# Kernel optimization log

Hardware: AMD Instinct MI355X
Metric: run time of the kernel (lower is better)

The kernel has to match this reference:

```python
import jax, jax.numpy as jnp
import numpy as np

D_MODEL = 1024
N_HEADS = 16
HEAD_DIM = D_MODEL // N_HEADS
D_FF = 4096
EPS = 1e-5


def layer_norm(x, w, b):
    mu = jnp.mean(x, axis=-1, keepdims=True)
    var = jnp.var(x, axis=-1, keepdims=True)
    return (x - mu) * jax.lax.rsqrt(var + EPS) * w + b


def setup_inputs() -> dict:
    key = jax.random.key(0)
    ks = jax.random.split(key, 8)
    B, T, C = 2, 2048, D_MODEL
    s = lambda fan_in: 1.0 / np.sqrt(fan_in)
    return {
        "x": jax.random.normal(ks[0], (B, T, C), dtype=jnp.float32),
        "ln1_w": jnp.ones((C,), jnp.float32),
        "ln1_b": jnp.zeros((C,), jnp.float32),
        "qkv_w": jax.random.normal(ks[1], (3 * C, C), jnp.float32) * s(C),
        "attn_out_w": jax.random.normal(ks[2], (C, C), jnp.float32) * s(C),
        "ln2_w": jnp.ones((C,), jnp.float32),
        "ln2_b": jnp.zeros((C,), jnp.float32),
        "mlp_in_w": jax.random.normal(ks[3], (D_FF, C), jnp.float32) * s(C),
        "mlp_gate_w": jax.random.normal(ks[4], (D_FF, C), jnp.float32) * s(C),
        "mlp_out_w": jax.random.normal(ks[5], (C, D_FF), jnp.float32) * s(D_FF),
    }


def reference(x, ln1_w, ln1_b, qkv_w, attn_out_w, ln2_w, ln2_b,
              mlp_in_w, mlp_gate_w, mlp_out_w):
    B, T, C = x.shape
    # --- causal self-attention (pre-norm) ---
    h = layer_norm(x, ln1_w, ln1_b)
    qkv = h @ qkv_w.T  # [B,T,3C]
    q, k, v = jnp.split(qkv, 3, axis=-1)
    def heads(t):
        return t.reshape(B, T, N_HEADS, HEAD_DIM).transpose(0, 2, 1, 3)  # [B,H,T,Dh]
    q, k, v = heads(q), heads(k), heads(v)
    scale = HEAD_DIM ** -0.5
    scores = jnp.einsum("bhqd,bhkd->bhqk", q, k) * scale  # [B,H,T,T]
    causal = jnp.tril(jnp.ones((T, T), dtype=bool))
    scores = jnp.where(causal, scores, -jnp.inf)
    attn = jax.nn.softmax(scores, axis=-1)
    out = jnp.einsum("bhqk,bhkd->bhqd", attn, v)
    out = out.transpose(0, 2, 1, 3).reshape(B, T, C)
    x = x + out @ attn_out_w.T
    # --- SwiGLU MLP (pre-norm) ---
    h = layer_norm(x, ln2_w, ln2_b)
    acts = jax.nn.silu(h @ mlp_in_w.T) * (h @ mlp_gate_w.T)
    return x + acts @ mlp_out_w.T
```

## Files before the change

### kernel.cpp

```cpp
#include <hip/hip_runtime.h>
#include <cstdint>

typedef unsigned short u16;
typedef __bf16 bf16x8 __attribute__((ext_vector_type(8)));
typedef float  f32x4  __attribute__((ext_vector_type(4)));

struct alignas(16) F4 { float v[4]; };
struct alignas(8)  U4 { u16 v[4]; };
struct alignas(16) U8 { u16 v[8]; };

__device__ __forceinline__ u16 f2bf(float f) {
    union { float f; unsigned int u; } x; x.f = f;
    unsigned int r = x.u + 0x7fffu + ((x.u >> 16) & 1u);
    return (u16)(r >> 16);
}
__device__ __forceinline__ float bf2f(u16 u) {
    union { unsigned int u; float f; } x; x.u = ((unsigned int)u) << 16;
    return x.f;
}
__device__ __forceinline__ f32x4 mfma16(bf16x8 a, bf16x8 b, f32x4 c) {
    return __builtin_amdgcn_mfma_f32_16x16x32_bf16(a, b, c, 0, 0, 0);
}
__device__ __forceinline__ bf16x8 ldf(const u16* p) { return *(const bf16x8*)p; }
__device__ __forceinline__ void gload_lds16(const void* g, void* l) {
    auto* gp = reinterpret_cast<const __attribute__((address_space(1))) unsigned int*>(
        reinterpret_cast<uintptr_t>(g));
    auto* lp = reinterpret_cast<__attribute__((address_space(3))) unsigned int*>(
        reinterpret_cast<uintptr_t>(l));
    __builtin_amdgcn_global_load_lds(gp, lp, 16, 0, 0);
}

__global__ __launch_bounds__(256) void cast_all_k(const float* __restrict__ qkvw,
                                                  const float* __restrict__ attow,
                                                  const float* __restrict__ mlpow,
                                                  const float* __restrict__ wi,
                                                  const float* __restrict__ wg,
                                                  u16* __restrict__ wq,
                                                  u16* __restrict__ wo,
                                                  u16* __restrict__ wm,
                                                  u16* __restrict__ wig) {
    constexpr int N1 = 3 * 1024 * 1024 / 8;
    constexpr int N2 = N1 + 1024 * 1024 / 8;
    constexpr int N3 = N2 + 1024 * 4096 / 8;
    const int i = blockIdx.x * 256 + threadIdx.x;
    const float* src; u16* dst;
    if (i < N1)      { src = qkvw  + (size_t)i * 8;        dst = wq + (size_t)i * 8; }
    else if (i < N2) { const int j = i - N1; src = attow + (size_t)j * 8; dst = wo + (size_t)j * 8; }
    else if (i < N3) { const int j = i - N2; src = mlpow + (size_t)j * 8; dst = wm + (size_t)j * 8; }
    else {
        const int j = i - N3;
        const int w = j >> 7, c8 = (j & 127) * 8;
        const int f = ((w >> 6) << 5) | (w & 31);
        src = ((w & 32) ? wg : wi) + (size_t)f * 1024 + c8;
        dst = wig + (size_t)w * 1024 + c8;
    }
    F4 a = *(const F4*)src;
    F4 b = *(const F4*)(src + 4);
    U8 o;
    #pragma unroll
    for (int j = 0; j < 4; ++j) { o.v[j] = f2bf(a.v[j]); o.v[4 + j] = f2bf(b.v[j]); }
    *(U8*)dst = o;
}

__global__ __launch_bounds__(256) void ln_fwd_k(const float* __restrict__ x,
                                                const float* __restrict__ w,
                                                const float* __restrict__ b,
                                                u16* __restrict__ h) {
    const int row = blockIdx.x, tid = threadIdx.x;
    const float* xr = x + (size_t)row * 1024;
    F4 v = *(const F4*)(xr + tid * 4);
    float s  = v.v[0] + v.v[1] + v.v[2] + v.v[3];
    float ss = v.v[0]*v.v[0] + v.v[1]*v.v[1] + v.v[2]*v.v[2] + v.v[3]*v.v[3];
    #pragma unroll
    for (int o = 32; o > 0; o >>= 1) { s += __shfl_down(s, o); ss += __shfl_down(ss, o); }
    __shared__ float red[8];
    const int wave = tid >> 6, lane = tid & 63;
    if (lane == 0) { red[wave] = s; red[4 + wave] = ss; }
    __syncthreads();
    s  = red[0] + red[1] + red[2] + red[3];
    ss = red[4] + red[5] + red[6] + red[7];
    const float mu   = s * (1.0f / 1024.0f);
    const float var  = ss * (1.0f / 1024.0f) - mu * mu;
    const float rstd = rsqrtf(var + 1e-5f);
    U4 o;
    #pragma unroll
    for (int j = 0; j < 4; ++j)
        o.v[j] = f2bf((v.v[j] - mu) * rstd * w[tid * 4 + j] + b[tid * 4 + j]);
    *(U4*)(h + (size_t)row * 1024 + tid * 4) = o;
}

__global__ __launch_bounds__(256) void ln_resid_k(const float* __restrict__ x,
                                                  const u16* __restrict__ p,
                                                  const float* __restrict__ w,
                                                  const float* __restrict__ b,
                                                  float* __restrict__ x1,
                                                  u16* __restrict__ h,
                                                  int planeEls) {
    const int row = blockIdx.x, tid = threadIdx.x;
    const size_t base = (size_t)row * 1024 + tid * 4;
    F4 xv = *(const F4*)(x + base);
    U4 q0 = *(const U4*)(p + base);
    U4 q1 = *(const U4*)(p + (size_t)planeEls + base);
    F4 sv;
    #pragma unroll
    for (int j = 0; j < 4; ++j) sv.v[j] = xv.v[j] + bf2f(q0.v[j]) + bf2f(q1.v[j]);
    *(F4*)(x1 + base) = sv;
    float s  = sv.v[0] + sv.v[1] + sv.v[2] + sv.v[3];
    float ss = sv.v[0]*sv.v[0] + sv.v[1]*sv.v[1] + sv.v[2]*sv.v[2] + sv.v[3]*sv.v[3];
    #pragma unroll
    for (int o = 32; o > 0; o >>= 1) { s += __shfl_down(s, o); ss += __shfl_down(ss, o); }
    __shared__ float red[8];
    const int wave = tid >> 6, lane = tid & 63;
    if (lane == 0) { red[wave] = s; red[4 + wave] = ss; }
    __syncthreads();
    s  = red[0] + red[1] + red[2] + red[3];
    ss = red[4] + red[5] + red[6] + red[7];
    const float mu   = s * (1.0f / 1024.0f);
    const float var  = ss * (1.0f / 1024.0f) - mu * mu;
    const float rstd = rsqrtf(var + 1e-5f);
    U4 o;
    #pragma unroll
    for (int j = 0; j < 4; ++j)
        o.v[j] = f2bf((sv.v[j] - mu) * rstd * w[tid * 4 + j] + b[tid * 4 + j]);
    *(U4*)(h + base) = o;
}

__global__ __launch_bounds__(256) void gemm_qkvt_k(const u16* __restrict__ h1,
                                                   const u16* __restrict__ wq,
                                                   u16* __restrict__ qk_b,
                                                   u16* __restrict__ vt_b) {
    __shared__ alignas(16) u16 Alds[128 * 32];
    __shared__ alignas(16) u16 Blds[128 * 32];
    const int tid  = threadIdx.x;
    const int lane = tid & 63, wave = tid >> 6;
    const int wr = wave >> 1, wc = wave & 1;
    const int r16 = lane & 15, g16 = lane >> 4;

    const u16* A; const u16* Bm; u16* Cout; int bn, bm, N, role;
    const int bid = blockIdx.x;
    if (bid < 512) { A = h1; Bm = wq; Cout = qk_b; N = 2048; bn = bid & 15; bm = bid >> 4; role = 0; }
    else {
        const int id = bid - 512;
        A = wq + (size_t)2 * 1024 * 1024;
        Bm = h1; Cout = vt_b; N = 4096; bn = id & 31; bm = id >> 5; role = 1;
    }
    constexpr int K = 1024;

    const int srow = lane >> 2;
    const int scol = (lane & 3) * 8;

    f32x4 acc[4][4] = {};

    for (int k0 = 0; k0 < K; k0 += 32) {
        #pragma unroll
        for (int c = 0; c < 2; ++c) {
            const int ch = wave * 2 + c;
            const u16* ga = A  + ((size_t)bm * 128 + ch * 16 + srow) * K + k0 + scol;
            gload_lds16(ga, &Alds[ch * 512]);
            const u16* gb = Bm + ((size_t)bn * 128 + ch * 16 + srow) * K + k0 + scol;
            gload_lds16(gb, &Blds[ch * 512]);
        }
        __syncthreads();
        bf16x8 af[4], bfr[4];
        #pragma unroll
        for (int m = 0; m < 4; ++m)
            af[m] = ldf(&Alds[(wr * 64 + m * 16 + r16) * 32 + g16 * 8]);
        #pragma unroll
        for (int n = 0; n < 4; ++n)
            bfr[n] = ldf(&Blds[(wc * 64 + n * 16 + r16) * 32 + g16 * 8]);
        #pragma unroll
        for (int m = 0; m < 4; ++m)
            #pragma unroll
            for (int n = 0; n < 4; ++n)
                acc[m][n] = mfma16(af[m], bfr[n], acc[m][n]);
        __syncthreads();
    }

    constexpr float SCQ = 0.125f * 1.44269504088896341f;
    #pragma unroll
    for (int m = 0; m < 4; ++m)
        #pragma unroll
        for (int n = 0; n < 4; ++n)
            #pragma unroll
            for (int r = 0; r < 4; ++r) {
                const int row = bm * 128 + wr * 64 + m * 16 + g16 * 4 + r;
                int col = bn * 128 + wc * 64 + n * 16 + r16;
                float v = acc[m][n][r];
                if (role == 0) {
                    if (col < 1024) v *= SCQ;
                } else {
                    const int c5 = col & 31;
                    const int pos = 8 * ((c5 & 15) >> 2) + 4 * (c5 >> 4) + (c5 & 3);
                    col = (col & ~31) | pos;
                }
                Cout[(size_t)row * N + col] = f2bf(v);
            }
}

__global__ __launch_bounds__(256) void gemm_btsplit_k(const u16* __restrict__ A,
                                                      const u16* __restrict__ Bm,
                                                      u16* __restrict__ P,
                                                      int N, int K, int kchunk,
                                                      int planeEls) {
    __shared__ alignas(16) u16 Alds[128 * 32];
    __shared__ alignas(16) u16 Blds[128 * 32];
    const int tid  = threadIdx.x;
    const int lane = tid & 63, wave = tid >> 6;
    const int wr = wave >> 1, wc = wave & 1;
    const int r16 = lane & 15, g16 = lane >> 4;
    const int bn = blockIdx.x, bm = blockIdx.y;
    const int kBeg = blockIdx.z * kchunk;

    const int srow = lane >> 2;
    const int scol = (lane & 3) * 8;

    f32x4 acc[4][4] = {};

    for (int k0 = kBeg; k0 < kBeg + kchunk; k0 += 32) {
        #pragma unroll
        for (int c = 0; c < 2; ++c) {
            const int ch = wave * 2 + c;
            const u16* ga = A  + ((size_t)bm * 128 + ch * 16 + srow) * K + k0 + scol;
            gload_lds16(ga, &Alds[ch * 512]);
            const u16* gb = Bm + ((size_t)bn * 128 + ch * 16 + srow) * K + k0 + scol;
            gload_lds16(gb, &Blds[ch * 512]);
        }
        __syncthreads();
        bf16x8 af[4], bfr[4];
        #pragma unroll
        for (int m = 0; m < 4; ++m)
            af[m] = ldf(&Alds[(wr * 64 + m * 16 + r16) * 32 + g16 * 8]);
        #pragma unroll
        for (int n = 0; n < 4; ++n)
            bfr[n] = ldf(&Blds[(wc * 64 + n * 16 + r16) * 32 + g16 * 8]);
        #pragma unroll
        for (int m = 0; m < 4; ++m)
            #pragma unroll
            for (int n = 0; n < 4; ++n)
                acc[m][n] = mfma16(af[m], bfr[n], acc[m][n]);
        __syncthreads();
    }

    u16* Pp = P + (size_t)blockIdx.z * planeEls;
    #pragma unroll
    for (int m = 0; m < 4; ++m)
        #pragma unroll
        for (int n = 0; n < 4; ++n)
            #pragma unroll
            for (int r = 0; r < 4; ++r) {
                const int row = bm * 128 + wr * 64 + m * 16 + g16 * 4 + r;
                const int col = bn * 128 + wc * 64 + n * 16 + r16;
                Pp[(size_t)row * N + col] = f2bf(acc[m][n][r]);
            }
}

template <int EPI>
__global__ __launch_bounds__(512, 2)
void gemm256_k(const u16* __restrict__ A, const u16* __restrict__ Bm,
               void* __restrict__ Cout, int lda, int ldb, int kLen,
               int nx, int bnCh, int outLd, int planeEls) {
    __shared__ alignas(16) u16 lds[2][2][2][128 * 64];

    const int tid  = threadIdx.x;
    const int wave = tid >> 6, lane = tid & 63;
    const int wm = wave >> 2, wn = wave & 3;
    const int r16 = lane & 15, g16 = lane >> 4;

    const int cpx = gridDim.x >> 3;
    const int xcd = blockIdx.x & 7, loc = blockIdx.x >> 3;
    const int mCh = cpx / bnCh;
    const int cpr = nx / bnCh;
    const int bm = (xcd / cpr) * mCh + loc / bnCh;
    const int bn = (xcd % cpr) * bnCh + loc % bnCh;
    const int kBeg = blockIdx.z * kLen;
    const int NT = kLen >> 6;

    const int csw = ((lane & 7) ^ (lane >> 3)) * 8;
    const u16* aU = A  + (size_t)(bm * 256) * lda + kBeg;
    const u16* bU = Bm + (size_t)(bn * 256) * ldb + kBeg;
    int aOff[2][2], bOff[2][2];
    #pragma unroll
    for (int h = 0; h < 2; ++h)
        #pragma unroll
        for (int i = 0; i < 2; ++i) {
            const int wr = wave * 16 + (lane >> 3) + i * 8;
            const int ar = (wr >> 6) * 128 + h * 64 + (wr & 63);
            const int br = (wr >> 5) * 64 + h * 32 + (wr & 31);
            aOff[h][i] = ar * lda + csw;
            bOff[h][i] = br * ldb + csw;
        }

    auto stA = [&](int kt, int h) {
        u16* d = &lds[kt & 1][0][h][wave * 1024];
        gload_lds16(aU + aOff[h][0] + kt * 64, d);
        gload_lds16(aU + aOff[h][1] + kt * 64, d + 512);
    };
    auto stB = [&](int kt, int h) {
        u16* d = &lds[kt & 1][1][h][wave * 1024];
        gload_lds16(bU + bOff[h][0] + kt * 64, d);
        gload_lds16(bU + bOff[h][1] + kt * 64, d + 512);
    };

    int offA[4][2], offB[2][2];
    #pragma unroll
    for (int m = 0; m < 4; ++m)
        #pragma unroll
        for (int ks = 0; ks < 2; ++ks)
            offA[m][ks] = (wm * 64 + m * 16 + r16) * 64 + (((ks * 4 + g16) ^ (r16 & 7)) * 8);
    #pragma unroll
    for (int n = 0; n < 2; ++n)
        #pragma unroll
        for (int ks = 0; ks < 2; ++ks)
            offB[n][ks] = (wn * 32 + n * 16 + r16) * 64 + (((ks * 4 + g16) ^ (r16 & 7)) * 8);

    f32x4 acc[8][4] = {};
    bf16x8 af0[4][2], af1[4][2], b0v[2][2], b1v[2][2];

    auto rdAF0 = [&](int buf) {
        const u16* P = &lds[buf][0][0][0];
        #pragma unroll
        for (int m = 0; m < 4; ++m) { af0[m][0] = ldf(P + offA[m][0]); af0[m][1] = ldf(P + offA[m][1]); }
    };
    auto rdAF1 = [&](int buf) {
        const u16* P = &lds[buf][0][1][0];
        #pragma unroll
        for (int m = 0; m < 4; ++m) { af1[m][0] = ldf(P + offA[m][0]); af1[m][1] = ldf(P + offA[m][1]); }
    };
    auto rdB0 = [&](int buf) {
        const u16* P = &lds[buf][1][0][0];
        #pragma unroll
        for (int n = 0; n < 2; ++n) { b0v[n][0] = ldf(P + offB[n][0]); b0v[n][1] = ldf(P + offB[n][1]); }
    };
    auto rdB1 = [&](int buf) {
        const u16* P = &lds[buf][1][1][0];
        #pragma unroll
        for (int n = 0; n < 2; ++n) { b1v[n][0] = ldf(P + offB[n][0]); b1v[n][1] = ldf(P + offB[n][1]); }
    };

    stA(0, 0); stB(0, 0); stB(0, 1); stA(0, 1);
    stA(1, 0); stB(1, 0); stB(1, 1); stA(1, 1);
    asm volatile("s_waitcnt vmcnt(8)" ::: "memory");
    __builtin_amdgcn_s_barrier();
    rdAF0(0); rdB0(0); rdB1(0); rdAF1(0);

    for (int kt = 0; kt < NT; ++kt) {
        const bool pf = (kt + 2 < NT);
        const int nb = (kt + 1) & 1;

        __builtin_amdgcn_s_setprio(1);
        #pragma unroll
        for (int m = 0; m < 4; ++m)
            #pragma unroll
            for (int n = 0; n < 2; ++n) {
                acc[m][n] = mfma16(af0[m][0], b0v[n][0], acc[m][n]);
                acc[m][n] = mfma16(af0[m][1], b0v[n][1], acc[m][n]);
            }
        __builtin_amdgcn_s_setprio(0);
        __builtin_amdgcn_s_barrier();

        if (pf) { stA(kt + 2, 0); stB(kt + 2, 0); }
        __builtin_amdgcn_s_setprio(1);
        #pragma unroll
        for (int m = 0; m < 4; ++m)
            #pragma unroll
            for (int n = 0; n < 2; ++n) {
                acc[m][n + 2] = mfma16(af0[m][0], b1v[n][0], acc[m][n + 2]);
                acc[m][n + 2] = mfma16(af0[m][1], b1v[n][1], acc[m][n + 2]);
            }
        __builtin_amdgcn_s_setprio(0);
        __builtin_amdgcn_s_barrier();

        if (pf) stB(kt + 2, 1);
        __builtin_amdgcn_s_setprio(1);
        #pragma unroll
        for (int m = 0; m < 4; ++m)
            #pragma unroll
            for (int n = 0; n < 2; ++n) {
                acc[m + 4][n] = mfma16(af1[m][0], b0v[n][0], acc[m + 4][n]);
                acc[m + 4][n] = mfma16(af1[m][1], b0v[n][1], acc[m + 4][n]);
            }
        __builtin_amdgcn_s_setprio(0);
        __builtin_amdgcn_s_barrier();

        if (pf) stA(kt + 2, 1);
        if (pf)               { asm volatile("s_waitcnt vmcnt(8)" ::: "memory"); }
        else if (kt + 1 < NT) { asm volatile("s_waitcnt vmcnt(0)" ::: "memory"); }
        if (kt + 1 < NT) {
            __builtin_amdgcn_s_barrier();
            rdAF0(nb); rdB0(nb);
        }
        __builtin_amdgcn_s_setprio(1);
        #pragma unroll
        for (int m = 0; m < 4; ++m)
            #pragma unroll
            for (int n = 0; n < 2; ++n) {
                acc[m + 4][n + 2] = mfma16(af1[m][0], b1v[n][0], acc[m + 4][n + 2]);
                acc[m + 4][n + 2] = mfma16(af1[m][1], b1v[n][1], acc[m + 4][n + 2]);
            }
        __builtin_amdgcn_s_setprio(0);
        if (kt + 1 < NT) { rdB1(nb); rdAF1(nb); }
    }

    if constexpr (EPI == 1) {
        u16* P = (u16*)Cout + (size_t)blockIdx.z * planeEls;
        #pragma unroll
        for (int m = 0; m < 8; ++m)
            #pragma unroll
            for (int n = 0; n < 4; ++n)
                #pragma unroll
                for (int r = 0; r < 4; ++r) {
                    const int row = bm * 256 + wm * 128 + m * 16 + g16 * 4 + r;
                    const int col = bn * 256 + wn * 64 + n * 16 + r16;
                    P[(size_t)row * outLd + col] = f2bf(acc[m][n][r]);
                }
    } else {
        (void)planeEls;
        u16* O = (u16*)Cout;
        #pragma unroll
        for (int m = 0; m < 8; ++m)
            #pragma unroll
            for (int n = 0; n < 2; ++n)
                #pragma unroll
                for (int r = 0; r < 4; ++r) {
                    const int row = bm * 256 + wm * 128 + m * 16 + g16 * 4 + r;
                    const int col = (bn * 4 + wn) * 32 + n * 16 + r16;
                    const float vi = acc[m][n][r];
                    const float vg = acc[m][n + 2][r];
                    const float sl = vi / (1.0f + __expf(-vi));
                    O[(size_t)row * outLd + col] = f2bf(sl * vg);
                }
    }
}

__global__ __launch_bounds__(256) void addreduce4_k(const float* __restrict__ resid,
                                                    const u16* __restrict__ p,
                                                    float* __restrict__ out,
                                                    int n4, int planeEls) {
    for (int i = blockIdx.x * 256 + threadIdx.x; i < n4; i += gridDim.x * 256) {
        F4 a = *(const F4*)(resid + (size_t)i * 4);
        U4 q0 = *(const U4*)(p + (size_t)i * 4);
        U4 q1 = *(const U4*)(p + (size_t)planeEls + (size_t)i * 4);
        U4 q2 = *(const U4*)(p + (size_t)2 * planeEls + (size_t)i * 4);
        U4 q3 = *(const U4*)(p + (size_t)3 * planeEls + (size_t)i * 4);
        F4 o;
        #pragma unroll
        for (int j = 0; j < 4; ++j)
            o.v[j] = a.v[j] + bf2f(q0.v[j]) + bf2f(q1.v[j]) + bf2f(q2.v[j]) + bf2f(q3.v[j]);
        *(F4*)(out + (size_t)i * 4) = o;
    }
}

__global__ __launch_bounds__(256) void attn_fwd_k(const u16* __restrict__ qk,
                                                  const u16* __restrict__ vt,
                                                  u16* __restrict__ Ob) {
    __shared__ alignas(16) u16 Klds[2][64 * 64];
    __shared__ alignas(16) u16 Vlds[2][64 * 64];

    const int tid  = threadIdx.x;
    const int wave = tid >> 6, lane = tid & 63;
    const int r16  = lane & 15, g16 = lane >> 4;

    const int bh = blockIdx.x >> 4, pi = blockIdx.x & 15;
    const int h  = bh & 15, b = bh >> 4;
    const size_t seqb = (size_t)b * 2048;

    const u16* kbase = qk + seqb * 2048 + 1024 + (size_t)h * 64;
    const u16* vbase = vt + (size_t)(h * 64) * 4096 + seqb;

    const int srow  = tid >> 3;
    const int scol8 = ((tid & 7) ^ (srow & 7)) * 8;
    const u16* ksrc = kbase + (size_t)srow * 2048 + scol8;
    const u16* vsrc = vbase + (size_t)srow * 4096 + scol8;

    auto stage = [&](int bufi, int kv0) {
        const u16* kp = ksrc + (size_t)kv0 * 2048;
        const u16* vp = vsrc + kv0;
        u16* kd = &Klds[bufi][wave * 512];
        u16* vd = &Vlds[bufi][wave * 512];
        gload_lds16(kp, kd);
        gload_lds16(kp + (size_t)32 * 2048, kd + 2048);
        gload_lds16(vp, vd);
        gload_lds16(vp + (size_t)32 * 4096, vd + 2048);
    };

    #pragma unroll 1
    for (int half = 0; half < 2; ++half) {
        const int qb  = half ? pi : (31 - pi);
        const int q0w = qb * 64 + wave * 16;

        const u16* qp = qk + (seqb + q0w + r16) * 2048 + h * 64 + g16 * 8;
        const bf16x8 qf0 = *(const bf16x8*)qp;
        const bf16x8 qf1 = *(const bf16x8*)(qp + 32);

        f32x4 o[4] = {};
        float mreg = -3.0e38f, lreg = 0.0f;
        const int nt = qb + 1;

        if (half) __syncthreads();
        stage(0, 0);
        asm volatile("s_waitcnt vmcnt(0)" ::: "memory");
        __builtin_amdgcn_s_barrier();

        for (int it = 0; it < nt; ++it) {
            const int kv0 = it * 64;
            const int cur = it & 1;
            if (it + 1 < nt) stage(cur ^ 1, kv0 + 64);

            const u16* K = Klds[cur];
            const u16* V = Vlds[cur];

            f32x4 s[4];
            #pragma unroll
            for (int t = 0; t < 4; ++t) {
                const int row = 16 * t + r16;
                const int sw  = row & 7;
                const bf16x8 k0 = ldf(&K[row * 64 + ((g16 ^ sw) * 8)]);
                const bf16x8 k1 = ldf(&K[row * 64 + (((g16 + 4) ^ sw) * 8)]);
                f32x4 acc = {0.f, 0.f, 0.f, 0.f};
                acc = mfma16(k0, qf0, acc);
                acc = mfma16(k1, qf1, acc);
                s[t] = acc;
            }

            float a[16];
            #pragma unroll
            for (int t = 0; t < 4; ++t)
                #pragma unroll
                for (int r = 0; r < 4; ++r) a[4 * t + r] = s[t][r];

            if (kv0 + 63 > q0w) {
                const int qg = q0w + r16;
                #pragma unroll
                for (int t = 0; t < 4; ++t)
                    #pragma unroll
                    for (int r = 0; r < 4; ++r)
                        if (kv0 + 16 * t + 4 * g16 + r > qg) a[4 * t + r] = -1.0e30f;
            }

            float mx = a[0];
            #pragma unroll
            for (int j = 1; j < 16; ++j) mx = fmaxf(mx, a[j]);
            mx = fmaxf(mx, __shfl_xor(mx, 16));
            mx = fmaxf(mx, __shfl_xor(mx, 32));

            const float mn = fmaxf(mreg, mx);
            float p[16], rs = 0.0f;
            #pragma unroll
            for (int j = 0; j < 16; ++j) { p[j] = exp2f(a[j] - mn); rs += p[j]; }
            rs += __shfl_xor(rs, 16);
            rs += __shfl_xor(rs, 32);

            if (__all(mx <= mreg)) {
                lreg += rs;
            } else {
                const float al = exp2f(mreg - mn);
                lreg = lreg * al + rs;
                mreg = mn;
                #pragma unroll
                for (int t = 0; t < 4; ++t)
                    #pragma unroll
                    for (int r = 0; r < 4; ++r) o[t][r] *= al;
            }

            bf16x8 pf0, pf1;
            #pragma unroll
            for (int j = 0; j < 8; ++j) { pf0[j] = (__bf16)p[j]; pf1[j] = (__bf16)p[8 + j]; }

            #pragma unroll
            for (int t = 0; t < 4; ++t) {
                const int row = 16 * t + r16;
                const int sw  = row & 7;
                const bf16x8 v0 = ldf(&V[row * 64 + ((g16 ^ sw) * 8)]);
                const bf16x8 v1 = ldf(&V[row * 64 + (((4 + g16) ^ sw) * 8)]);
                o[t] = mfma16(v0, pf0, o[t]);
                o[t] = mfma16(v1, pf1, o[t]);
            }

            if (it + 1 < nt) {
                asm volatile("s_waitcnt vmcnt(0)" ::: "memory");
                __builtin_amdgcn_s_barrier();
            }
        }

        const float inv = 1.0f / lreg;
        u16* op = Ob + (seqb + q0w + r16) * 1024 + h * 64 + 4 * g16;
        #pragma unroll
        for (int t = 0; t < 4; ++t) {
            U4 st;
            #pragma unroll
            for (int r = 0; r < 4; ++r) st.v[r] = f2bf(o[t][r] * inv);
            *(U4*)(op + 16 * t) = st;
        }
    }
}

extern "C" void kernel_launch(void* const* d_in, const int* in_sizes, int n_in,
                              void* d_out, int out_size, void* d_ws, size_t ws_size,
                              hipStream_t stream) {
    (void)in_sizes; (void)n_in; (void)out_size; (void)ws_size;
    constexpr int C = 1024, FF = 4096, M = 2 * 2048;
    constexpr size_t MB = 1024 * 1024;

    const float* x      = (const float*)d_in[0];
    const float* ln1_w  = (const float*)d_in[1];
    const float* ln1_b  = (const float*)d_in[2];
    const float* qkv_w  = (const float*)d_in[3];
    const float* atto_w = (const float*)d_in[4];
    const float* ln2_w  = (const float*)d_in[5];
    const float* ln2_b  = (const float*)d_in[6];
    const float* mlpi_w = (const float*)d_in[7];
    const float* mlpg_w = (const float*)d_in[8];
    const float* mlpo_w = (const float*)d_in[9];
    float* out = (float*)d_out;

    char* ws = (char*)d_ws;
    size_t off = 0;
    auto alloc = [&](size_t bytes) {
        char* p = ws + off;
        off += (bytes + 255) & ~(size_t)255;
        return p;
    };
    u16*   wq   = (u16*)  alloc((size_t)3 * C * C * 2);
    u16*   wo   = (u16*)  alloc((size_t)C * C * 2);
    u16*   wig  = (u16*)  alloc((size_t)2 * FF * C * 2);
    u16*   wm   = (u16*)  alloc((size_t)C * FF * 2);
    float* x1   = (float*)alloc((size_t)M * C * 4);
    u16*   h2   = (u16*)  alloc((size_t)M * C * 2);
    u16*   ab   = (u16*)  alloc((size_t)M * FF * 2);
    char*  R    = alloc(64 * MB);
    u16*   h1   = (u16*)R;
    u16*   qk_b = (u16*)(R + 8 * MB);
    u16*   vt_b = (u16*)(R + 24 * MB);
    u16*   Ob   = (u16*)(R + 32 * MB);
    u16*   aoP  = (u16*)(R + 40 * MB);
    u16*   pscr = (u16*)R;

    cast_all_k<<<8192, 256, 0, stream>>>(qkv_w, atto_w, mlpo_w, mlpi_w, mlpg_w,
                                         wq, wo, wm, wig);

    ln_fwd_k<<<M, 256, 0, stream>>>(x, ln1_w, ln1_b, h1);
    gemm_qkvt_k<<<768, 256, 0, stream>>>(h1, wq, qk_b, vt_b);
    attn_fwd_k<<<512, 256, 0, stream>>>(qk_b, vt_b, Ob);
    gemm_btsplit_k<<<dim3(C / 128, M / 128, 2), 256, 0, stream>>>(
        Ob, wo, aoP, C, C, C / 2, M * C);
    ln_resid_k<<<M, 256, 0, stream>>>(x, aoP, ln2_w, ln2_b, x1, h2, M * C);

    gemm256_k<2><<<dim3((2 * FF / 256) * (M / 256), 1, 1), 512, 0, stream>>>(
        h2, wig, ab, C, C, C, 2 * FF / 256, 8, FF, 0);
    gemm256_k<1><<<dim3((C / 256) * (M / 256), 1, 4), 512, 0, stream>>>(
        ab, wm, pscr, FF, FF, FF / 4, C / 256, 4, C, M * C);
    addreduce4_k<<<2048, 256, 0, stream>>>(x1, pscr, out, M * C / 4, M * C);
}
```

Before: 244.1 us.

## Simplify 256x256 GEMM to K=32 double-buffered loop and split MLP-out K eight ways

Replaces the hand-interleaved 4-phase K=64 pipeline in the 256x256 GEMM with a simpler K=32 stage loop. It prefetches the next stage while computing the current one and issues all 32 MFMAs per step. Separately, the MLP down-projection split-K goes from 4 to 8 planes, with an 8-plane reduce kernel, to raise block count. The trade-off is a barrier and full vmcnt(0) wait every 32 K, less LDS reuse per sync, and more partial-sum traffic in the reduce.

```diff
diff --git a/kernel.cpp b/kernel.cpp
--- a/kernel.cpp
+++ b/kernel.cpp
@@ -259,7 +259,7 @@
 void gemm256_k(const u16* __restrict__ A, const u16* __restrict__ Bm,
                void* __restrict__ Cout, int lda, int ldb, int kLen,
                int nx, int bnCh, int outLd, int planeEls) {
-    __shared__ alignas(16) u16 lds[2][2][2][128 * 64];
+    __shared__ alignas(16) u16 lds[2][2][8192];
 
     const int tid  = threadIdx.x;
     const int wave = tid >> 6, lane = tid & 63;
@@ -273,136 +273,74 @@
     const int bm = (xcd / cpr) * mCh + loc / bnCh;
     const int bn = (xcd % cpr) * bnCh + loc % bnCh;
     const int kBeg = blockIdx.z * kLen;
-    const int NT = kLen >> 6;
-
-    const int csw = ((lane & 7) ^ (lane >> 3)) * 8;
+    const int P = kLen >> 5;
+
     const u16* aU = A  + (size_t)(bm * 256) * lda + kBeg;
     const u16* bU = Bm + (size_t)(bn * 256) * ldb + kBeg;
-    int aOff[2][2], bOff[2][2];
-    #pragma unroll
-    for (int h = 0; h < 2; ++h)
-        #pragma unroll
-        for (int i = 0; i < 2; ++i) {
-            const int wr = wave * 16 + (lane >> 3) + i * 8;
-            const int ar = (wr >> 6) * 128 + h * 64 + (wr & 63);
-            const int br = (wr >> 5) * 64 + h * 32 + (wr & 31);
-            aOff[h][i] = ar * lda + csw;
-            bOff[h][i] = br * ldb + csw;
+    int aOf[2], bOf[2];
+    #pragma unroll
+    for (int i = 0; i < 2; ++i) {
+        const int q = tid + i * 512;
+        const int row = q >> 2;
+        const int sc = (q & 3) ^ ((q >> 3) & 3);
+        aOf[i] = row * lda + sc * 8;
+        bOf[i] = row * ldb + sc * 8;
+    }
+
+    auto stage = [&](int p) {
+        const int s = p & 1;
+        const int ko = p * 32;
+        u16* dA = &lds[s][0][wave * 512];
+        u16* dB = &lds[s][1][wave * 512];
+        gload_lds16(aU + aOf[0] + ko, dA);
+        gload_lds16(aU + aOf[1] + ko, dA + 4096);
+        gload_lds16(bU + bOf[0] + ko, dB);
+        gload_lds16(bU + bOf[1] + ko, dB + 4096);
+    };
+
+    int offA[8], offB[4];
+    #pragma unroll
+    for (int m = 0; m < 8; ++m) {
+        const int r = wm * 128 + m * 16 + r16;
+        offA[m] = r * 32 + ((g16 ^ ((r >> 1) & 3)) * 8);
+    }
+    #pragma unroll
+    for (int n = 0; n < 4; ++n) {
+        const int r = wn * 64 + n * 16 + r16;
+        offB[n] = r * 32 + ((g16 ^ ((r >> 1) & 3)) * 8);
+    }
+
+    f32x4 acc[8][4] = {};
+
+    stage(0);
+    asm volatile("s_waitcnt vmcnt(0)" ::: "memory");
+    __builtin_amdgcn_s_barrier();
+
+    for (int p = 0; p < P; ++p) {
+        const int s = p & 1;
+        if (p + 1 < P) stage(p + 1);
+        bf16x8 af[8], bfr[4];
+        const u16* PA = &lds[s][0][0];
+        const u16* PB = &lds[s][1][0];
+        #pragma unroll
+        for (int m = 0; m < 8; ++m) af[m] = ldf(PA + offA[m]);
+        #pragma unroll
+        for (int n = 0; n < 4; ++n) bfr[n] = ldf(PB + offB[n]);
+        __builtin_amdgcn_s_setprio(1);
+        #pragma unroll
+        for (int m = 0; m < 8; ++m)
+            #pragma unroll
+            for (int n = 0; n < 4; ++n)
+                acc[m][n] = mfma16(af[m], bfr[n], acc[m][n]);
+        __builtin_amdgcn_s_setprio(0);
+        if (p + 1 < P) {
+            asm volatile("s_waitcnt vmcnt(0)" ::: "memory");
+            __builtin_amdgcn_s_barrier();
         }
-
-    auto stA = [&](int kt, int h) {
-        u16* d = &lds[kt & 1][0][h][wave * 1024];
-        gload_lds16(aU + aOff[h][0] + kt * 64, d);
-        gload_lds16(aU + aOff[h][1] + kt * 64, d + 512);
-    };
-    auto stB = [&](int kt, int h) {
-        u16* d = &lds[kt & 1][1][h][wave * 1024];
-        gload_lds16(bU + bOff[h][0] + kt * 64, d);
-        gload_lds16(bU + bOff[h][1] + kt * 64, d + 512);
-    };
-
-    int offA[4][2], offB[2][2];
-    #pragma unroll
-    for (int m = 0; m < 4; ++m)
-        #pragma unroll
-        for (int ks = 0; ks < 2; ++ks)
-            offA[m][ks] = (wm * 64 + m * 16 + r16) * 64 + (((ks * 4 + g16) ^ (r16 & 7)) * 8);
-    #pragma unroll
-    for (int n = 0; n < 2; ++n)
-        #pragma unroll
-        for (int ks = 0; ks < 2; ++ks)
-            offB[n][ks] = (wn * 32 + n * 16 + r16) * 64 + (((ks * 4 + g16) ^ (r16 & 7)) * 8);
-
-    f32x4 acc[8][4] = {};
-    bf16x8 af0[4][2], af1[4][2], b0v[2][2], b1v[2][2];
-
-    auto rdAF0 = [&](int buf) {
-        const u16* P = &lds[buf][0][0][0];
-        #pragma unroll
-        for (int m = 0; m < 4; ++m) { af0[m][0] = ldf(P + offA[m][0]); af0[m][1] = ldf(P + offA[m][1]); }
-    };
-    auto rdAF1 = [&](int buf) {
-        const u16* P = &lds[buf][0][1][0];
-        #pragma unroll
-        for (int m = 0; m < 4; ++m) { af1[m][0] = ldf(P + offA[m][0]); af1[m][1] = ldf(P + offA[m][1]); }
-    };
-    auto rdB0 = [&](int buf) {
-        const u16* P = &lds[buf][1][0][0];
-        #pragma unroll
-        for (int n = 0; n < 2; ++n) { b0v[n][0] = ldf(P + offB[n][0]); b0v[n][1] = ldf(P + offB[n][1]); }
-    };
-    auto rdB1 = [&](int buf) {
-        const u16* P = &lds[buf][1][1][0];
-        #pragma unroll
-        for (int n = 0; n < 2; ++n) { b1v[n][0] = ldf(P + offB[n][0]); b1v[n][1] = ldf(P + offB[n][1]); }
-    };
-
-    stA(0, 0); stB(0, 0); stB(0, 1); stA(0, 1);
-    stA(1, 0); stB(1, 0); stB(1, 1); stA(1, 1);
-    asm volatile("s_waitcnt vmcnt(8)" ::: "memory");
-    __builtin_amdgcn_s_barrier();
-    rdAF0(0); rdB0(0); rdB1(0); rdAF1(0);
-
-    for (int kt = 0; kt < NT; ++kt) {
-        const bool pf = (kt + 2 < NT);
-        const int nb = (kt + 1) & 1;
-
-        __builtin_amdgcn_s_setprio(1);
-        #pragma unroll
-        for (int m = 0; m < 4; ++m)
-            #pragma unroll
-            for (int n = 0; n < 2; ++n) {
-                acc[m][n] = mfma16(af0[m][0], b0v[n][0], acc[m][n]);
-                acc[m][n] = mfma16(af0[m][1], b0v[n][1], acc[m][n]);
-            }
-        __builtin_amdgcn_s_setprio(0);
-        __builtin_amdgcn_s_barrier();
-
-        if (pf) { stA(kt + 2, 0); stB(kt + 2, 0); }
-        __builtin_amdgcn_s_setprio(1);
-        #pragma unroll
-        for (int m = 0; m < 4; ++m)
-            #pragma unroll
-            for (int n = 0; n < 2; ++n) {
-                acc[m][n + 2] = mfma16(af0[m][0], b1v[n][0], acc[m][n + 2]);
-                acc[m][n + 2] = mfma16(af0[m][1], b1v[n][1], acc[m][n + 2]);
-            }
-        __builtin_amdgcn_s_setprio(0);
-        __builtin_amdgcn_s_barrier();
-
-        if (pf) stB(kt + 2, 1);
-        __builtin_amdgcn_s_setprio(1);
-        #pragma unroll
-        for (int m = 0; m < 4; ++m)
-            #pragma unroll
-            for (int n = 0; n < 2; ++n) {
-                acc[m + 4][n] = mfma16(af1[m][0], b0v[n][0], acc[m + 4][n]);
-                acc[m + 4][n] = mfma16(af1[m][1], b0v[n][1], acc[m + 4][n]);
-            }
-        __builtin_amdgcn_s_setprio(0);
-        __builtin_amdgcn_s_barrier();
-
-        if (pf) stA(kt + 2, 1);
-        if (pf)               { asm volatile("s_waitcnt vmcnt(8)" ::: "memory"); }
-        else if (kt + 1 < NT) { asm volatile("s_waitcnt vmcnt(0)" ::: "memory"); }
-        if (kt + 1 < NT) {
-            __builtin_amdgcn_s_barrier();
-            rdAF0(nb); rdB0(nb);
-        }
-        __builtin_amdgcn_s_setprio(1);
-        #pragma unroll
-        for (int m = 0; m < 4; ++m)
-            #pragma unroll
-            for (int n = 0; n < 2; ++n) {
-                acc[m + 4][n + 2] = mfma16(af1[m][0], b1v[n][0], acc[m + 4][n + 2]);
-                acc[m + 4][n + 2] = mfma16(af1[m][1], b1v[n][1], acc[m + 4][n + 2]);
-            }
-        __builtin_amdgcn_s_setprio(0);
-        if (kt + 1 < NT) { rdB1(nb); rdAF1(nb); }
     }
 
     if constexpr (EPI == 1) {
-        u16* P = (u16*)Cout + (size_t)blockIdx.z * planeEls;
+        u16* Pp = (u16*)Cout + (size_t)blockIdx.z * planeEls;
         #pragma unroll
         for (int m = 0; m < 8; ++m)
             #pragma unroll
@@ -411,7 +349,7 @@
                 for (int r = 0; r < 4; ++r) {
                     const int row = bm * 256 + wm * 128 + m * 16 + g16 * 4 + r;
                     const int col = bn * 256 + wn * 64 + n * 16 + r16;
-                    P[(size_t)row * outLd + col] = f2bf(acc[m][n][r]);
+                    Pp[(size_t)row * outLd + col] = f2bf(acc[m][n][r]);
                 }
     } else {
         (void)planeEls;
@@ -432,20 +370,19 @@
     }
 }
 
-__global__ __launch_bounds__(256) void addreduce4_k(const float* __restrict__ resid,
+__global__ __launch_bounds__(256) void addreduce8_k(const float* __restrict__ resid,
                                                     const u16* __restrict__ p,
                                                     float* __restrict__ out,
                                                     int n4, int planeEls) {
     for (int i = blockIdx.x * 256 + threadIdx.x; i < n4; i += gridDim.x * 256) {
         F4 a = *(const F4*)(resid + (size_t)i * 4);
-        U4 q0 = *(const U4*)(p + (size_t)i * 4);
-        U4 q1 = *(const U4*)(p + (size_t)planeEls + (size_t)i * 4);
-        U4 q2 = *(const U4*)(p + (size_t)2 * planeEls + (size_t)i * 4);
-        U4 q3 = *(const U4*)(p + (size_t)3 * planeEls + (size_t)i * 4);
-        F4 o;
-        #pragma unroll
-        for (int j = 0; j < 4; ++j)
-            o.v[j] = a.v[j] + bf2f(q0.v[j]) + bf2f(q1.v[j]) + bf2f(q2.v[j]) + bf2f(q3.v[j]);
+        F4 o = a;
+        #pragma unroll
+        for (int pl = 0; pl < 8; ++pl) {
+            U4 q = *(const U4*)(p + (size_t)pl * planeEls + (size_t)i * 4);
+            #pragma unroll
+            for (int j = 0; j < 4; ++j) o.v[j] += bf2f(q.v[j]);
+        }
         *(F4*)(out + (size_t)i * 4) = o;
     }
 }
@@ -647,7 +584,7 @@
 
     gemm256_k<2><<<dim3((2 * FF / 256) * (M / 256), 1, 1), 512, 0, stream>>>(
         h2, wig, ab, C, C, C, 2 * FF / 256, 8, FF, 0);
-    gemm256_k<1><<<dim3((C / 256) * (M / 256), 1, 4), 512, 0, stream>>>(
-        ab, wm, pscr, FF, FF, FF / 4, C / 256, 4, C, M * C);
-    addreduce4_k<<<2048, 256, 0, stream>>>(x1, pscr, out, M * C / 4, M * C);
-}
+    gemm256_k<1><<<dim3((C / 256) * (M / 256), 1, 8), 512, 0, stream>>>(
+        ab, wm, pscr, FF, FF, FF / 8, C / 256, 4, C, M * C);
+    addreduce8_k<<<2048, 256, 0, stream>>>(x1, pscr, out, M * C / 4, M * C);
+}
```

Result: slower. 264.9 us (+8.5%).

## Restructure GEMM main loop to prefetch one tile ahead with fewer fragment registers

Applied to the files above, without the earlier changes.

The GEMM main loop changes from prefetching two k-tiles ahead, with A fragments for both halves held in registers, to prefetching one tile ahead. It reuses a single A fragment array that is reloaded from LDS between quadrants. This cuts VGPR pressure, which may allow more occupancy or avoid spills. In exchange it adds extra barriers, lgkmcnt waits before each MFMA group, and less latency hiding for global loads.

```diff
diff --git a/kernel.cpp b/kernel.cpp
--- a/kernel.cpp
+++ b/kernel.cpp
@@ -314,91 +314,89 @@
             offB[n][ks] = (wn * 32 + n * 16 + r16) * 64 + (((ks * 4 + g16) ^ (r16 & 7)) * 8);
 
     f32x4 acc[8][4] = {};
-    bf16x8 af0[4][2], af1[4][2], b0v[2][2], b1v[2][2];
-
-    auto rdAF0 = [&](int buf) {
-        const u16* P = &lds[buf][0][0][0];
-        #pragma unroll
-        for (int m = 0; m < 4; ++m) { af0[m][0] = ldf(P + offA[m][0]); af0[m][1] = ldf(P + offA[m][1]); }
-    };
-    auto rdAF1 = [&](int buf) {
-        const u16* P = &lds[buf][0][1][0];
-        #pragma unroll
-        for (int m = 0; m < 4; ++m) { af1[m][0] = ldf(P + offA[m][0]); af1[m][1] = ldf(P + offA[m][1]); }
-    };
-    auto rdB0 = [&](int buf) {
-        const u16* P = &lds[buf][1][0][0];
-        #pragma unroll
-        for (int n = 0; n < 2; ++n) { b0v[n][0] = ldf(P + offB[n][0]); b0v[n][1] = ldf(P + offB[n][1]); }
-    };
-    auto rdB1 = [&](int buf) {
-        const u16* P = &lds[buf][1][1][0];
-        #pragma unroll
-        for (int n = 0; n < 2; ++n) { b1v[n][0] = ldf(P + offB[n][0]); b1v[n][1] = ldf(P + offB[n][1]); }
-    };
+    bf16x8 af[4][2], b0v[2][2], b1v[2][2];
 
     stA(0, 0); stB(0, 0); stB(0, 1); stA(0, 1);
-    stA(1, 0); stB(1, 0); stB(1, 1); stA(1, 1);
-    asm volatile("s_waitcnt vmcnt(8)" ::: "memory");
+    asm volatile("s_waitcnt vmcnt(4)" ::: "memory");
     __builtin_amdgcn_s_barrier();
-    rdAF0(0); rdB0(0); rdB1(0); rdAF1(0);
 
     for (int kt = 0; kt < NT; ++kt) {
-        const bool pf = (kt + 2 < NT);
-        const int nb = (kt + 1) & 1;
-
+        const int b = kt & 1;
+        const bool pf = (kt + 1 < NT);
+        const u16* A0 = &lds[b][0][0][0];
+        const u16* A1 = &lds[b][0][1][0];
+        const u16* B0 = &lds[b][1][0][0];
+        const u16* B1 = &lds[b][1][1][0];
+
+        #pragma unroll
+        for (int m = 0; m < 4; ++m) { af[m][0] = ldf(A0 + offA[m][0]); af[m][1] = ldf(A0 + offA[m][1]); }
+        #pragma unroll
+        for (int n = 0; n < 2; ++n) { b0v[n][0] = ldf(B0 + offB[n][0]); b0v[n][1] = ldf(B0 + offB[n][1]); }
+        if (pf) stA(kt + 1, 0);
+        __builtin_amdgcn_s_barrier();
+        asm volatile("s_waitcnt lgkmcnt(0)" ::: "memory");
         __builtin_amdgcn_s_setprio(1);
         #pragma unroll
         for (int m = 0; m < 4; ++m)
             #pragma unroll
             for (int n = 0; n < 2; ++n) {
-                acc[m][n] = mfma16(af0[m][0], b0v[n][0], acc[m][n]);
-                acc[m][n] = mfma16(af0[m][1], b0v[n][1], acc[m][n]);
+                acc[m][n] = mfma16(af[m][0], b0v[n][0], acc[m][n]);
+                acc[m][n] = mfma16(af[m][1], b0v[n][1], acc[m][n]);
             }
         __builtin_amdgcn_s_setprio(0);
-        __builtin_amdgcn_s_barrier();
-
-        if (pf) { stA(kt + 2, 0); stB(kt + 2, 0); }
+        if (pf) { asm volatile("s_waitcnt vmcnt(4)" ::: "memory"); }
+        else    { asm volatile("s_waitcnt vmcnt(2)" ::: "memory"); }
+        __builtin_amdgcn_s_barrier();
+
+        #pragma unroll
+        for (int n = 0; n < 2; ++n) { b1v[n][0] = ldf(B1 + offB[n][0]); b1v[n][1] = ldf(B1 + offB[n][1]); }
+        if (pf) stB(kt + 1, 0);
+        __builtin_amdgcn_s_barrier();
+        asm volatile("s_waitcnt lgkmcnt(0)" ::: "memory");
         __builtin_amdgcn_s_setprio(1);
         #pragma unroll
         for (int m = 0; m < 4; ++m)
             #pragma unroll
             for (int n = 0; n < 2; ++n) {
-                acc[m][n + 2] = mfma16(af0[m][0], b1v[n][0], acc[m][n + 2]);
-                acc[m][n + 2] = mfma16(af0[m][1], b1v[n][1], acc[m][n + 2]);
+                acc[m][n + 2] = mfma16(af[m][0], b1v[n][0], acc[m][n + 2]);
+                acc[m][n + 2] = mfma16(af[m][1], b1v[n][1], acc[m][n + 2]);
             }
         __builtin_amdgcn_s_setprio(0);
-        __builtin_amdgcn_s_barrier();
-
-        if (pf) stB(kt + 2, 1);
+        if (pf) { asm volatile("s_waitcnt vmcnt(4)" ::: "memory"); }
+        else    { asm volatile("s_waitcnt vmcnt(0)" ::: "memory"); }
+        __builtin_amdgcn_s_barrier();
+
+        #pragma unroll
+        for (int m = 0; m < 4; ++m) { af[m][0] = ldf(A1 + offA[m][0]); af[m][1] = ldf(A1 + offA[m][1]); }
+        if (pf) stB(kt + 1, 1);
+        __builtin_amdgcn_s_barrier();
+        asm volatile("s_waitcnt lgkmcnt(0)" ::: "memory");
         __builtin_amdgcn_s_setprio(1);
         #pragma unroll
         for (int m = 0; m < 4; ++m)
             #pragma unroll
             for (int n = 0; n < 2; ++n) {
-                acc[m + 4][n] = mfma16(af1[m][0], b0v[n][0], acc[m + 4][n]);
-                acc[m + 4][n] = mfma16(af1[m][1], b0v[n][1], acc[m + 4][n]);
+                acc[m + 4][n] = mfma16(af[m][0], b0v[n][0], acc[m + 4][n]);
+                acc[m + 4][n] = mfma16(af[m][1], b0v[n][1], acc[m + 4][n]);
             }
         __builtin_amdgcn_s_setprio(0);
         __builtin_amdgcn_s_barrier();
 
-        if (pf) stA(kt + 2, 1);
-        if (pf)               { asm volatile("s_waitcnt vmcnt(8)" ::: "memory"); }
-        else if (kt + 1 < NT) { asm volatile("s_waitcnt vmcnt(0)" ::: "memory"); }
-        if (kt + 1 < NT) {
+        if (pf) stA(kt + 1, 1);
+        __builtin_amdgcn_s_barrier();
+        __builtin_amdgcn_s_setprio(1);
+        #pragma unroll
+        for (int m = 0; m < 4; ++m)
+            #pragma unroll
+            for (int n = 0; n < 2; ++n) {
+                acc[m + 4][n + 2] = mfma16(af[m][0], b1v[n][0], acc[m + 4][n + 2]);
+                acc[m + 4][n + 2] = mfma16(af[m][1], b1v[n][1], acc[m + 4][n + 2]);
+            }
+        __builtin_amdgcn_s_setprio(0);
+        if (pf) {
+            asm volatile("s_waitcnt vmcnt(4)" ::: "memory");
             __builtin_amdgcn_s_barrier();
-            rdAF0(nb); rdB0(nb);
         }
-        __builtin_amdgcn_s_setprio(1);
-        #pragma unroll
-        for (int m = 0; m < 4; ++m)
-            #pragma unroll
-            for (int n = 0; n < 2; ++n) {
-                acc[m + 4][n + 2] = mfma16(af1[m][0], b1v[n][0], acc[m + 4][n + 2]);
-                acc[m + 4][n + 2] = mfma16(af1[m][1], b1v[n][1], acc[m + 4][n + 2]);
-            }
-        __builtin_amdgcn_s_setprio(0);
-        if (kt + 1 < NT) { rdB1(nb); rdAF1(nb); }
     }
 
     if constexpr (EPI == 1) {
```

Result: slower. 251.3 us (+3.0%).
